# Kernel tuning notes

Hardware: AMD Instinct MI355X
Metric: run time of the kernel (lower is better)

The kernel has to match this reference:

```python
import jax, jax.numpy as jnp
import numpy as np

H = 512  # hidden_size

def setup_inputs() -> dict:
    key = jax.random.key(0)
    ks = jax.random.split(key, 5)
    B, S = 2, 512
    feats = jax.random.normal(ks[0], (B, S, H), dtype=jnp.float32)
    # torch Linear init ~ U(-1/sqrt(in), 1/sqrt(in)); scaled normals are fine for a reference
    W1 = jax.random.normal(ks[1], (2 * H, H), dtype=jnp.float32) / np.sqrt(2 * H)
    b1 = jnp.zeros((H,), dtype=jnp.float32)
    W2 = jax.random.normal(ks[2], (H, H // 2), dtype=jnp.float32) / np.sqrt(H)
    b2 = jnp.zeros((H // 2,), dtype=jnp.float32)
    W3 = jax.random.normal(ks[3], (H // 2, 1), dtype=jnp.float32) / np.sqrt(H // 2)
    b3 = jnp.zeros((1,), dtype=jnp.float32)
    return {"features": feats, "W1": W1, "b1": b1, "W2": W2, "b2": b2, "W3": W3, "b3": b3}


def reference(features, W1, b1, W2, b2, W3, b3):
    # cat([f_i, f_j]) @ W1 == f_i @ W1[:H] + f_j @ W1[H:]
    # Precompute the two halves once per residue instead of per pair.
    a = jnp.einsum('bsh,hk->bsk', features, W1[:H])          # [B,S,H]
    c = jnp.einsum('bsh,hk->bsk', features, W1[H:])          # [B,S,H]
    h1 = jax.nn.relu(a[:, :, None, :] + c[:, None, :, :] + b1)  # [B,S,S,H]
    # Dropout(0.1) is identity at inference.
    h2 = jax.nn.relu(jnp.einsum('bijh,hk->bijk', h1, W2) + b2)  # [B,S,S,H//2]
    logits = jnp.einsum('bijk,ko->bijo', h2, W3) + b3            # [B,S,S,1]
    return jax.nn.sigmoid(logits[..., 0])                        # [B,S,S]
```

## Files before the change

kernel.cpp:

```cpp
#include <hip/hip_runtime.h>

#define S_DIM 512
#define H_DIM 512
#define NH 256
#define TI 16
#define TJ 8
#define SROW 520

#define AS1 __attribute__((address_space(1)))
#define AS3 __attribute__((address_space(3)))

typedef _Float16 half8 __attribute__((ext_vector_type(8)));
typedef float f32x16 __attribute__((ext_vector_type(16)));

__global__ __launch_bounds__(256) void convert_w2_kernel(const float* __restrict__ W2,
                                                         _Float16* __restrict__ w2L) {
    int t = blockIdx.x * 256 + threadIdx.x;
    int gcb = t >> 8, n = t & 255;
    half8 v;
#pragma unroll
    for (int j = 0; j < 8; j++) v[j] = (_Float16)W2[(size_t)(gcb * 8 + j) * NH + n];
    *(half8*)&w2L[((size_t)gcb * 256 + n) * 8] = v;
}

__global__ __launch_bounds__(128) void prep_mfma_kernel(const float* __restrict__ feats,
        const float* __restrict__ W1, const float* __restrict__ b1,
        _Float16* __restrict__ aH, _Float16* __restrict__ cH) {
    const int tid = threadIdx.x, wave = tid >> 6, lane = tid & 63;
    const int m32 = lane & 31, ch = lane >> 5;
    const int m0 = blockIdx.y * 32;
    const int n = blockIdx.x * 64 + wave * 32 + m32;
    const bool fh = (n < H_DIM);
    const float* wcol = fh ? &W1[n] : &W1[(size_t)H_DIM * H_DIM + (n - H_DIM)];
    const float* arow = &feats[(size_t)(m0 + m32) * H_DIM + ch * 8];

    f32x16 acc = (f32x16)0.f;
#pragma unroll
    for (int ks = 0; ks < 32; ks++) {
        const int kbase = ks * 16 + ch * 8;
        float4 a0 = *(const float4*)&arow[ks * 16];
        float4 a1 = *(const float4*)&arow[ks * 16 + 4];
        half8 af, bf;
        af[0] = (_Float16)a0.x; af[1] = (_Float16)a0.y;
        af[2] = (_Float16)a0.z; af[3] = (_Float16)a0.w;
        af[4] = (_Float16)a1.x; af[5] = (_Float16)a1.y;
        af[6] = (_Float16)a1.z; af[7] = (_Float16)a1.w;
#pragma unroll
        for (int j = 0; j < 8; j++) bf[j] = (_Float16)wcol[(size_t)(kbase + j) * H_DIM];
        acc = __builtin_amdgcn_mfma_f32_32x32x16_f16(af, bf, acc, 0, 0, 0);
    }
    const float bias = fh ? b1[n] : 0.f;
#pragma unroll
    for (int r = 0; r < 16; r++) {
        int m = m0 + (r & 3) + 8 * (r >> 2) + 4 * ch;
        float v = acc[r] + bias;
        if (fh) aH[(size_t)m * H_DIM + n] = (_Float16)v;
        else    cH[(size_t)m * H_DIM + (n - H_DIM)] = (_Float16)v;
    }
}

__global__ __launch_bounds__(512, 4) void pair_kernel(
        const _Float16* __restrict__ aH, const _Float16* __restrict__ cH,
        const _Float16* __restrict__ w2L,
        const float* __restrict__ b2, const float* __restrict__ W3,
        const float* __restrict__ b3, float* __restrict__ out) {
    const int jt = blockIdx.x, it = blockIdx.y, b = blockIdx.z;
    const int i0 = it * TI, j0 = jt * TJ;

    __shared__ __align__(16) _Float16 sa[TI * SROW];
    __shared__ __align__(16) _Float16 sc[TJ * SROW];
    __shared__ float spart[2 * 64 * 32];

    const int tid = threadIdx.x;
    const int wave = tid >> 6, lane = tid & 63;
    const int mg = wave >> 2, ng = wave & 3;
    const int nb = ng * 64;
    const int m32 = lane & 31, ch = lane >> 5;

#pragma unroll
    for (int rr0 = 0; rr0 < 3; rr0++) {
        int rr = rr0 * 8 + wave;
        if (rr < TI) {
            __builtin_amdgcn_global_load_lds(
                (const AS1 unsigned int*)&aH[((size_t)(b * S_DIM + i0 + rr)) * H_DIM + lane * 8],
                (AS3 unsigned int*)&sa[rr * SROW], 16, 0, 0);
        } else {
            int cr = rr - TI;
            __builtin_amdgcn_global_load_lds(
                (const AS1 unsigned int*)&cH[((size_t)(b * S_DIM + j0 + cr)) * H_DIM + lane * 8],
                (AS3 unsigned int*)&sc[cr * SROW], 16, 0, 0);
        }
    }

    const int il0 = mg * 8 + (m32 >> 3);
    const int il1 = il0 + 4;
    const int jl = m32 & 7;
    const _Float16* vaB0 = &sa[il0 * SROW + ch * 8];
    const _Float16* vaB1 = &sa[il1 * SROW + ch * 8];
    const _Float16* vcB  = &sc[jl * SROW + ch * 8];

    f32x16 acc[2][2];
#pragma unroll
    for (int mt = 0; mt < 2; mt++)
#pragma unroll
        for (int nt = 0; nt < 2; nt++) acc[mt][nt] = (f32x16)0.f;

    const _Float16* bp = &w2L[((size_t)ch * 256 + nb + m32) * 8];
    half8 bB[2][2];
    bB[0][0] = *(const half8*)&bp[0];
    bB[0][1] = *(const half8*)&bp[256];
    bB[1][0] = *(const half8*)&bp[4096];
    bB[1][1] = *(const half8*)&bp[4096 + 256];

    __syncthreads();

    half8 aB[2][3];
    aB[0][0] = *(const half8*)&vaB0[0];
    aB[0][1] = *(const half8*)&vaB1[0];
    aB[0][2] = *(const half8*)&vcB[0];

#pragma unroll
    for (int ks = 0; ks < 32; ks++) {
        const int cur = ks & 1, nxt = cur ^ 1;
        if (ks < 31) {
            aB[nxt][0] = *(const half8*)&vaB0[(ks + 1) * 16];
            aB[nxt][1] = *(const half8*)&vaB1[(ks + 1) * 16];
            aB[nxt][2] = *(const half8*)&vcB[(ks + 1) * 16];
        }
        half8 bf0 = bB[cur][0], bf1 = bB[cur][1];
        if (ks < 30) {
            const _Float16* bn = bp + (size_t)(ks + 2) * 4096;
            bB[cur][0] = *(const half8*)&bn[0];
            bB[cur][1] = *(const half8*)&bn[256];
        }
        half8 af0 = __builtin_elementwise_max(aB[cur][0] + aB[cur][2], (half8)(_Float16)0.f);
        half8 af1 = __builtin_elementwise_max(aB[cur][1] + aB[cur][2], (half8)(_Float16)0.f);
        acc[0][0] = __builtin_amdgcn_mfma_f32_32x32x16_f16(af0, bf0, acc[0][0], 0, 0, 0);
        acc[0][1] = __builtin_amdgcn_mfma_f32_32x32x16_f16(af0, bf1, acc[0][1], 0, 0, 0);
        acc[1][0] = __builtin_amdgcn_mfma_f32_32x32x16_f16(af1, bf0, acc[1][0], 0, 0, 0);
        acc[1][1] = __builtin_amdgcn_mfma_f32_32x32x16_f16(af1, bf1, acc[1][1], 0, 0, 0);
    }

    float b2v[2], w3v[2];
#pragma unroll
    for (int nt = 0; nt < 2; nt++) {
        int n = nb + nt * 32 + m32;
        b2v[nt] = b2[n];
        w3v[nt] = W3[n];
    }
#pragma unroll
    for (int mt = 0; mt < 2; mt++)
#pragma unroll
        for (int r = 0; r < 16; r++) {
            float s = 0.f;
#pragma unroll
            for (int nt = 0; nt < 2; nt++) {
                float v = acc[mt][nt][r] + b2v[nt];
                v = v > 0.f ? v : 0.f;
                s += v * w3v[nt];
            }
            s += __shfl_xor(s, 8);
            s += __shfl_xor(s, 16);
            if (m32 < 8) {
                int row = mt * 32 + (r & 3) + 8 * (r >> 2) + 4 * ch;
                int col = ng * 8 + m32;
                spart[mg * 2048 + row * 32 + ((col + row) & 31)] = s;
            }
        }
    __syncthreads();
    {
        const int R = tid >> 2, sub = tid & 3;
        const int mgf = R >> 6, rowf = R & 63;
        const float* base = &spart[mgf * 2048 + rowf * 32];
        float s = 0.f;
#pragma unroll
        for (int k = 0; k < 8; k++) s += base[(sub * 8 + k + rowf) & 31];
        s += __shfl_xor(s, 1);
        s += __shfl_xor(s, 2);
        if (sub == 0) {
            float tot = s + b3[0];
            float sg = 1.f / (1.f + __expf(-tot));
            int i = i0 + (R >> 3), j = j0 + (R & 7);
            out[(size_t)b * S_DIM * S_DIM + (size_t)i * S_DIM + j] = sg;
        }
    }
}

extern "C" void kernel_launch(void* const* d_in, const int* in_sizes, int n_in,
                              void* d_out, int out_size, void* d_ws, size_t ws_size,
                              hipStream_t stream) {
    const float* feats = (const float*)d_in[0];
    const float* W1 = (const float*)d_in[1];
    const float* b1 = (const float*)d_in[2];
    const float* W2 = (const float*)d_in[3];
    const float* b2 = (const float*)d_in[4];
    const float* W3 = (const float*)d_in[5];
    const float* b3 = (const float*)d_in[6];
    float* out = (float*)d_out;

    const int B = in_sizes[0] / (S_DIM * H_DIM);

    char* ws = (char*)d_ws;
    _Float16* aH   = (_Float16*)ws;
    _Float16* cH   = (_Float16*)(ws + (1 << 20));
    _Float16* w2L  = (_Float16*)(ws + (2 << 20));

    convert_w2_kernel<<<64, 256, 0, stream>>>(W2, w2L);
    prep_mfma_kernel<<<dim3(16, 32), 128, 0, stream>>>(feats, W1, b1, aH, cH);
    pair_kernel<<<dim3(S_DIM / TJ, S_DIM / TI, B), 512, 0, stream>>>(aH, cH, w2L, b2, W3, b3, out);
}
```

Baseline: 234.4 us.

## Make pair kernel persistent over j-tiles with double-buffered LDS and merge prep kernels

Measured after the change: 605.5 us. 2.58x slower.

```diff
diff --git a/kernel.cpp b/kernel.cpp
--- a/kernel.cpp
+++ b/kernel.cpp
@@ -3,8 +3,6 @@
 #define S_DIM 512
 #define H_DIM 512
 #define NH 256
-#define TI 16
-#define TJ 8
 #define SROW 520
 
 #define AS1 __attribute__((address_space(1)))
@@ -13,23 +11,26 @@
 typedef _Float16 half8 __attribute__((ext_vector_type(8)));
 typedef float f32x16 __attribute__((ext_vector_type(16)));
 
-__global__ __launch_bounds__(256) void convert_w2_kernel(const float* __restrict__ W2,
-                                                         _Float16* __restrict__ w2L) {
-    int t = blockIdx.x * 256 + threadIdx.x;
-    int gcb = t >> 8, n = t & 255;
-    half8 v;
-#pragma unroll
-    for (int j = 0; j < 8; j++) v[j] = (_Float16)W2[(size_t)(gcb * 8 + j) * NH + n];
-    *(half8*)&w2L[((size_t)gcb * 256 + n) * 8] = v;
-}
-
-__global__ __launch_bounds__(128) void prep_mfma_kernel(const float* __restrict__ feats,
+__global__ __launch_bounds__(256) void prep_kernel(const float* __restrict__ feats,
         const float* __restrict__ W1, const float* __restrict__ b1,
-        _Float16* __restrict__ aH, _Float16* __restrict__ cH) {
-    const int tid = threadIdx.x, wave = tid >> 6, lane = tid & 63;
+        const float* __restrict__ W2,
+        _Float16* __restrict__ aH, _Float16* __restrict__ cH, _Float16* __restrict__ w2L) {
+    const int blk = blockIdx.x;
+    const int tid = threadIdx.x;
+    if (blk >= 256) {
+        int t = (blk - 256) * 256 + tid;
+        int gcb = t >> 8, n = t & 255;
+        half8 v;
+#pragma unroll
+        for (int j = 0; j < 8; j++) v[j] = (_Float16)W2[(size_t)(gcb * 8 + j) * NH + n];
+        *(half8*)&w2L[((size_t)gcb * 256 + n) * 8] = v;
+        return;
+    }
+    const int wave = tid >> 6, lane = tid & 63;
     const int m32 = lane & 31, ch = lane >> 5;
-    const int m0 = blockIdx.y * 32;
-    const int n = blockIdx.x * 64 + wave * 32 + m32;
+    const int mg = wave >> 1, ng = wave & 1;
+    const int m0 = (blk >> 4) * 64 + mg * 32;
+    const int n = (blk & 15) * 64 + ng * 32 + m32;
     const bool fh = (n < H_DIM);
     const float* wcol = fh ? &W1[n] : &W1[(size_t)H_DIM * H_DIM + (n - H_DIM)];
     const float* arow = &feats[(size_t)(m0 + m32) * H_DIM + ch * 8];
@@ -64,11 +65,14 @@
         const _Float16* __restrict__ w2L,
         const float* __restrict__ b2, const float* __restrict__ W3,
         const float* __restrict__ b3, float* __restrict__ out) {
-    const int jt = blockIdx.x, it = blockIdx.y, b = blockIdx.z;
-    const int i0 = it * TI, j0 = jt * TJ;
-
-    __shared__ __align__(16) _Float16 sa[TI * SROW];
-    __shared__ __align__(16) _Float16 sc[TJ * SROW];
+    const int p = blockIdx.x;
+    const int g = p >> 3, q = p & 7;
+    const int b = g >> 5, it = g & 31;
+    const int i0 = it * 16;
+    const int jbase = q * 64;
+
+    __shared__ __align__(16) _Float16 sa[16 * SROW];
+    __shared__ __align__(16) _Float16 sc2[2][8 * SROW];
     __shared__ float spart[2 * 64 * 32];
 
     const int tid = threadIdx.x;
@@ -77,69 +81,21 @@
     const int nb = ng * 64;
     const int m32 = lane & 31, ch = lane >> 5;
 
-#pragma unroll
-    for (int rr0 = 0; rr0 < 3; rr0++) {
-        int rr = rr0 * 8 + wave;
-        if (rr < TI) {
-            __builtin_amdgcn_global_load_lds(
-                (const AS1 unsigned int*)&aH[((size_t)(b * S_DIM + i0 + rr)) * H_DIM + lane * 8],
-                (AS3 unsigned int*)&sa[rr * SROW], 16, 0, 0);
-        } else {
-            int cr = rr - TI;
-            __builtin_amdgcn_global_load_lds(
-                (const AS1 unsigned int*)&cH[((size_t)(b * S_DIM + j0 + cr)) * H_DIM + lane * 8],
-                (AS3 unsigned int*)&sc[cr * SROW], 16, 0, 0);
-        }
-    }
+    __builtin_amdgcn_global_load_lds(
+        (const AS1 unsigned int*)&aH[((size_t)(b * S_DIM + i0 + wave)) * H_DIM + lane * 8],
+        (AS3 unsigned int*)&sa[wave * SROW], 16, 0, 0);
+    __builtin_amdgcn_global_load_lds(
+        (const AS1 unsigned int*)&aH[((size_t)(b * S_DIM + i0 + wave + 8)) * H_DIM + lane * 8],
+        (AS3 unsigned int*)&sa[(wave + 8) * SROW], 16, 0, 0);
+    __builtin_amdgcn_global_load_lds(
+        (const AS1 unsigned int*)&cH[((size_t)(b * S_DIM + jbase + wave)) * H_DIM + lane * 8],
+        (AS3 unsigned int*)&sc2[0][wave * SROW], 16, 0, 0);
 
     const int il0 = mg * 8 + (m32 >> 3);
     const int il1 = il0 + 4;
     const int jl = m32 & 7;
     const _Float16* vaB0 = &sa[il0 * SROW + ch * 8];
     const _Float16* vaB1 = &sa[il1 * SROW + ch * 8];
-    const _Float16* vcB  = &sc[jl * SROW + ch * 8];
-
-    f32x16 acc[2][2];
-#pragma unroll
-    for (int mt = 0; mt < 2; mt++)
-#pragma unroll
-        for (int nt = 0; nt < 2; nt++) acc[mt][nt] = (f32x16)0.f;
-
-    const _Float16* bp = &w2L[((size_t)ch * 256 + nb + m32) * 8];
-    half8 bB[2][2];
-    bB[0][0] = *(const half8*)&bp[0];
-    bB[0][1] = *(const half8*)&bp[256];
-    bB[1][0] = *(const half8*)&bp[4096];
-    bB[1][1] = *(const half8*)&bp[4096 + 256];
-
-    __syncthreads();
-
-    half8 aB[2][3];
-    aB[0][0] = *(const half8*)&vaB0[0];
-    aB[0][1] = *(const half8*)&vaB1[0];
-    aB[0][2] = *(const half8*)&vcB[0];
-
-#pragma unroll
-    for (int ks = 0; ks < 32; ks++) {
-        const int cur = ks & 1, nxt = cur ^ 1;
-        if (ks < 31) {
-            aB[nxt][0] = *(const half8*)&vaB0[(ks + 1) * 16];
-            aB[nxt][1] = *(const half8*)&vaB1[(ks + 1) * 16];
-            aB[nxt][2] = *(const half8*)&vcB[(ks + 1) * 16];
-        }
-        half8 bf0 = bB[cur][0], bf1 = bB[cur][1];
-        if (ks < 30) {
-            const _Float16* bn = bp + (size_t)(ks + 2) * 4096;
-            bB[cur][0] = *(const half8*)&bn[0];
-            bB[cur][1] = *(const half8*)&bn[256];
-        }
-        half8 af0 = __builtin_elementwise_max(aB[cur][0] + aB[cur][2], (half8)(_Float16)0.f);
-        half8 af1 = __builtin_elementwise_max(aB[cur][1] + aB[cur][2], (half8)(_Float16)0.f);
-        acc[0][0] = __builtin_amdgcn_mfma_f32_32x32x16_f16(af0, bf0, acc[0][0], 0, 0, 0);
-        acc[0][1] = __builtin_amdgcn_mfma_f32_32x32x16_f16(af0, bf1, acc[0][1], 0, 0, 0);
-        acc[1][0] = __builtin_amdgcn_mfma_f32_32x32x16_f16(af1, bf0, acc[1][0], 0, 0, 0);
-        acc[1][1] = __builtin_amdgcn_mfma_f32_32x32x16_f16(af1, bf1, acc[1][1], 0, 0, 0);
-    }
 
     float b2v[2], w3v[2];
 #pragma unroll
@@ -148,40 +104,92 @@
         b2v[nt] = b2[n];
         w3v[nt] = W3[n];
     }
-#pragma unroll
-    for (int mt = 0; mt < 2; mt++)
-#pragma unroll
-        for (int r = 0; r < 16; r++) {
-            float s = 0.f;
-#pragma unroll
-            for (int nt = 0; nt < 2; nt++) {
-                float v = acc[mt][nt][r] + b2v[nt];
-                v = v > 0.f ? v : 0.f;
-                s += v * w3v[nt];
+    const float b3v = b3[0];
+
+    __syncthreads();
+
+#pragma unroll 1
+    for (int s = 0; s < 8; s++) {
+        const int cur = s & 1;
+        if (s < 7) {
+            __builtin_amdgcn_global_load_lds(
+                (const AS1 unsigned int*)
+                    &cH[((size_t)(b * S_DIM + jbase + (s + 1) * 8 + wave & 0x7fffffff)) * H_DIM + lane * 8],
+                (AS3 unsigned int*)&sc2[cur ^ 1][wave * SROW], 16, 0, 0);
+        }
+        const _Float16* vcB = &sc2[cur][jl * SROW + ch * 8];
+
+        f32x16 acc[2][2];
+#pragma unroll
+        for (int mt = 0; mt < 2; mt++)
+#pragma unroll
+            for (int nt = 0; nt < 2; nt++) acc[mt][nt] = (f32x16)0.f;
+
+        const _Float16* bp = &w2L[((size_t)ch * 256 + nb + m32) * 8];
+        half8 bB[2][2];
+        bB[0][0] = *(const half8*)&bp[0];
+        bB[0][1] = *(const half8*)&bp[256];
+        bB[1][0] = *(const half8*)&bp[4096];
+        bB[1][1] = *(const half8*)&bp[4096 + 256];
+
+#pragma unroll
+        for (int ks = 0; ks < 32; ks++) {
+            const int curk = ks & 1;
+            half8 bf0 = bB[curk][0], bf1 = bB[curk][1];
+            if (ks < 30) {
+                const _Float16* bn = bp + (size_t)(ks + 2) * 4096;
+                bB[curk][0] = *(const half8*)&bn[0];
+                bB[curk][1] = *(const half8*)&bn[256];
             }
-            s += __shfl_xor(s, 8);
-            s += __shfl_xor(s, 16);
-            if (m32 < 8) {
-                int row = mt * 32 + (r & 3) + 8 * (r >> 2) + 4 * ch;
-                int col = ng * 8 + m32;
-                spart[mg * 2048 + row * 32 + ((col + row) & 31)] = s;
+            half8 vc  = *(const half8*)&vcB[ks * 16];
+            half8 va0 = *(const half8*)&vaB0[ks * 16];
+            half8 va1 = *(const half8*)&vaB1[ks * 16];
+            half8 af0 = __builtin_elementwise_max(va0 + vc, (half8)(_Float16)0.f);
+            half8 af1 = __builtin_elementwise_max(va1 + vc, (half8)(_Float16)0.f);
+            acc[0][0] = __builtin_amdgcn_mfma_f32_32x32x16_f16(af0, bf0, acc[0][0], 0, 0, 0);
+            acc[0][1] = __builtin_amdgcn_mfma_f32_32x32x16_f16(af0, bf1, acc[0][1], 0, 0, 0);
+            acc[1][0] = __builtin_amdgcn_mfma_f32_32x32x16_f16(af1, bf0, acc[1][0], 0, 0, 0);
+            acc[1][1] = __builtin_amdgcn_mfma_f32_32x32x16_f16(af1, bf1, acc[1][1], 0, 0, 0);
+        }
+
+        __syncthreads();
+
+#pragma unroll
+        for (int mt = 0; mt < 2; mt++)
+#pragma unroll
+            for (int r = 0; r < 16; r++) {
+                float sv = 0.f;
+#pragma unroll
+                for (int nt = 0; nt < 2; nt++) {
+                    float v = acc[mt][nt][r] + b2v[nt];
+                    v = v > 0.f ? v : 0.f;
+                    sv += v * w3v[nt];
+                }
+                sv += __shfl_xor(sv, 8);
+                sv += __shfl_xor(sv, 16);
+                if (m32 < 8) {
+                    int row = mt * 32 + (r & 3) + 8 * (r >> 2) + 4 * ch;
+                    int col = ng * 8 + m32;
+                    spart[mg * 2048 + row * 32 + ((col + row) & 31)] = sv;
+                }
             }
-        }
-    __syncthreads();
-    {
-        const int R = tid >> 2, sub = tid & 3;
-        const int mgf = R >> 6, rowf = R & 63;
-        const float* base = &spart[mgf * 2048 + rowf * 32];
-        float s = 0.f;
-#pragma unroll
-        for (int k = 0; k < 8; k++) s += base[(sub * 8 + k + rowf) & 31];
-        s += __shfl_xor(s, 1);
-        s += __shfl_xor(s, 2);
-        if (sub == 0) {
-            float tot = s + b3[0];
-            float sg = 1.f / (1.f + __expf(-tot));
-            int i = i0 + (R >> 3), j = j0 + (R & 7);
-            out[(size_t)b * S_DIM * S_DIM + (size_t)i * S_DIM + j] = sg;
+        __syncthreads();
+
+        {
+            const int R = tid >> 2, sub = tid & 3;
+            const int mgf = R >> 6, rowf = R & 63;
+            const float* base = &spart[mgf * 2048 + rowf * 32];
+            float sv = 0.f;
+#pragma unroll
+            for (int k = 0; k < 8; k++) sv += base[(sub * 8 + k + rowf) & 31];
+            sv += __shfl_xor(sv, 1);
+            sv += __shfl_xor(sv, 2);
+            if (sub == 0) {
+                float tot = sv + b3v;
+                float sg = 1.f / (1.f + __expf(-tot));
+                int i = i0 + (R >> 3), j = jbase + s * 8 + (R & 7);
+                out[(size_t)b * S_DIM * S_DIM + (size_t)i * S_DIM + j] = sg;
+            }
         }
     }
 }
@@ -198,14 +206,11 @@
     const float* b3 = (const float*)d_in[6];
     float* out = (float*)d_out;
 
-    const int B = in_sizes[0] / (S_DIM * H_DIM);
-
     char* ws = (char*)d_ws;
     _Float16* aH   = (_Float16*)ws;
     _Float16* cH   = (_Float16*)(ws + (1 << 20));
     _Float16* w2L  = (_Float16*)(ws + (2 << 20));
 
-    convert_w2_kernel<<<64, 256, 0, stream>>>(W2, w2L);
-    prep_mfma_kernel<<<dim3(16, 32), 128, 0, stream>>>(feats, W1, b1, aH, cH);
-    pair_kernel<<<dim3(S_DIM / TJ, S_DIM / TI, B), 512, 0, stream>>>(aH, cH, w2L, b2, W3, b3, out);
+    prep_kernel<<<320, 256, 0, stream>>>(feats, W1, b1, W2, aH, cH, w2L);
+    pair_kernel<<<512, 512, 0, stream>>>(aH, cH, w2L, b2, W3, b3, out);
 }
```
